# Performance work log

Measured on AMD Instinct MI355X. Metric: run time of the kernel, lower is better.

The kernel has to match this reference:

```python
import jax, jax.numpy as jnp
import numpy as np

P_DROP = 0.1
NTYPES = 8
DROP_KEY = jax.random.key(42)


def _dropout(h, i):
    # deterministic training-mode dropout, mask fixed by layer index
    keep = jax.random.bernoulli(jax.random.fold_in(DROP_KEY, i), 1.0 - P_DROP, h.shape)
    return jnp.where(keep, h / (1.0 - P_DROP), 0.0).astype(h.dtype)


def _func_conv(h, src, dst, types, convW, convb, act):
    # gather src features along edges, mean-aggregate onto dst nodes,
    # then apply a per-gate-type linear transform.
    n_out = types.shape[0]
    msg = h[src]                                                  # [E, d]
    agg = jax.ops.segment_sum(msg, dst, num_segments=n_out)       # [n_out, d]
    deg = jax.ops.segment_sum(jnp.ones((src.shape[0],), h.dtype), dst,
                              num_segments=n_out)
    agg = agg / jnp.maximum(deg, 1.0)[:, None]
    out = jnp.zeros((n_out, convW.shape[2]), h.dtype)
    for t in range(convW.shape[0]):                                # ntypes is small & fixed
        mask = (types == t).astype(h.dtype)[:, None]
        out = out + (agg * mask) @ convW[t]
    out = out + convb[types]
    return jax.nn.relu(out) if act else out


def setup_inputs() -> dict:
    key = jax.random.key(0)
    ks = jax.random.split(key, 16)
    N0, N1, N2, N3 = 400_000, 200_000, 100_000, 50_000
    E0, E1, E2 = 1_600_000, 800_000, 400_000
    d, dout = 128, 64
    inp = {
        "features": jax.random.normal(ks[0], (N0, d), jnp.float32),
        "src0": jax.random.randint(ks[1], (E0,), 0, N0),
        "dst0": jax.random.randint(ks[2], (E0,), 0, N1),
        "types1": jax.random.randint(ks[3], (N1,), 0, NTYPES),
        "src1": jax.random.randint(ks[4], (E1,), 0, N1),
        "dst1": jax.random.randint(ks[5], (E1,), 0, N2),
        "types2": jax.random.randint(ks[6], (N2,), 0, NTYPES),
        "src2": jax.random.randint(ks[7], (E2,), 0, N2),
        "dst2": jax.random.randint(ks[8], (E2,), 0, N3),
        "types3": jax.random.randint(ks[9], (N3,), 0, NTYPES),
        # learned params
        "convW": jax.random.normal(ks[10], (NTYPES, d, d), jnp.float32) / np.sqrt(d),
        "convb": jnp.zeros((NTYPES, d), jnp.float32),
        "fcW": jax.random.normal(ks[11], (d, dout), jnp.float32) / np.sqrt(d),
        "fcb": jnp.zeros((dout,), jnp.float32),
    }
    return inp


def reference(features, src0, dst0, types1, src1, dst1, types2,
              src2, dst2, types3, convW, convb, fcW, fcb):
    blocks = [(src0, dst0, types1), (src1, dst1, types2), (src2, dst2, types3)]
    depth = len(blocks)
    h = features
    for i, (s, dst, t) in enumerate(blocks):
        if i != 0:
            h = _dropout(h, i)
        h = _func_conv(h, s, dst, t, convW, convb, act=(i != depth - 1))
    h = h @ fcW + fcb   # hidden_dim != out_dim -> fc_out applied
    return h            # squeeze(1) is a no-op for out_dim > 1
```

## Files before the change

### kernel.cpp

```cpp
#include <hip/hip_runtime.h>
#include <cstdint>
#include <cstddef>

__host__ __device__ inline void tf2x32(uint32_t k0, uint32_t k1,
                                       uint32_t x0, uint32_t x1,
                                       uint32_t* o0, uint32_t* o1)
{
    uint32_t ks2 = k0 ^ k1 ^ 0x1BD11BDAu;
    x0 += k0; x1 += k1;
#define TF_R(r) do { x0 += x1; x1 = (x1 << (r)) | (x1 >> (32 - (r))); x1 ^= x0; } while (0)
    TF_R(13); TF_R(15); TF_R(26); TF_R(6);
    x0 += k1;  x1 += ks2 + 1u;
    TF_R(17); TF_R(29); TF_R(16); TF_R(24);
    x0 += ks2; x1 += k0 + 2u;
    TF_R(13); TF_R(15); TF_R(26); TF_R(6);
    x0 += k0;  x1 += k1 + 3u;
    TF_R(17); TF_R(29); TF_R(16); TF_R(24);
    x0 += k1;  x1 += ks2 + 4u;
    TF_R(13); TF_R(15); TF_R(26); TF_R(6);
    x0 += ks2; x1 += k0 + 5u;
#undef TF_R
    *o0 = x0; *o1 = x1;
}

__device__ inline float drop_scale(uint32_t fk0, uint32_t fk1, uint32_t idx)
{
    uint32_t o0, o1;
    tf2x32(fk0, fk1, 0u, idx, &o0, &o1);
    uint32_t bits = o0 ^ o1;
    float u = __uint_as_float((bits >> 9) | 0x3f800000u) - 1.0f;
    return (u < 0.9f) ? (1.0f / 0.9f) : 0.0f;
}

__device__ inline ushort bf16_rn(float f)
{
    uint32_t u = __float_as_uint(f);
    u += 0x7fffu + ((u >> 16) & 1u);
    return (ushort)(u >> 16);
}
__device__ inline float bf16_f(ushort h) { return __uint_as_float(((uint32_t)h) << 16); }
__device__ inline uint32_t pack2bf(float a, float b)
{
    return (uint32_t)bf16_rn(a) | ((uint32_t)bf16_rn(b) << 16);
}
__device__ inline float bflo(uint32_t u) { return __uint_as_float(u << 16); }
__device__ inline float bfhi(uint32_t u) { return __uint_as_float(u & 0xffff0000u); }

typedef __attribute__((ext_vector_type(8))) short bf16x8;
typedef __attribute__((ext_vector_type(4))) float f32x4;

__global__ __launch_bounds__(256) void fcvt_kernel(
    const float4* __restrict__ in, uint2* __restrict__ out, long long n4)
{
    long long stride = (long long)gridDim.x * 256;
    for (long long i = blockIdx.x * 256LL + threadIdx.x; i < n4; i += stride) {
        float4 v = in[i];
        out[i] = make_uint2(pack2bf(v.x, v.y), pack2bf(v.z, v.w));
    }
}

__global__ __launch_bounds__(256) void prep_all_kernel(
    const float* __restrict__ convW, const float* __restrict__ convb,
    const float* __restrict__ fcW, const float* __restrict__ fcb,
    ushort* __restrict__ WThi, ushort* __restrict__ WTlo,
    ushort* __restrict__ WfThi, ushort* __restrict__ WfTlo,
    float* __restrict__ bfb)
{
    __shared__ float F[128 * 64];
    int t = blockIdx.x, tid = threadIdx.x;
    #pragma unroll
    for (int it = 0; it < 8; ++it) {
        int idx4 = (it * 256 + tid) * 4;
        *(float4*)&F[idx4] = *(const float4*)&fcW[idx4];
    }
    __syncthreads();

    {
        const float* S = convW + (size_t)t * 16384;
        ushort* DH = WThi + (size_t)t * 16384;
        ushort* DL = WTlo + (size_t)t * 16384;
        for (int idx = tid; idx < 16384; idx += 256) {
            int k = idx >> 7, c = idx & 127;
            float v = S[idx];
            ushort hi = bf16_rn(v);
            ushort lo = bf16_rn(v - bf16_f(hi));
            int pos = c * 128 + ((((k >> 3) ^ (c & 15)) << 3) | (k & 7));
            DH[pos] = hi; DL[pos] = lo;
        }
    }

    {
        int r = tid >> 1, cb = (tid & 1) * 32;
        const float* Wrow = convW + (size_t)t * 16384 + (size_t)r * 128;
        float acc[32];
        #pragma unroll
        for (int c = 0; c < 32; ++c) acc[c] = 0.f;
        for (int k = 0; k < 128; ++k) {
            float w = Wrow[k];
            #pragma unroll
            for (int c = 0; c < 32; ++c) acc[c] += w * F[k * 64 + cb + c];
        }
        ushort* FH = WfThi + (size_t)t * 8192;
        ushort* FL = WfTlo + (size_t)t * 8192;
        int swzr = (r & 7);
        #pragma unroll
        for (int c = 0; c < 32; ++c) {
            int col = cb + c;
            float v = acc[c];
            ushort hi = bf16_rn(v);
            ushort lo = bf16_rn(v - bf16_f(hi));
            int pos = col * 128 + ((((r >> 3) ^ (col & 15)) << 3) | swzr);
            FH[pos] = hi; FL[pos] = lo;
        }
    }

    if (tid < 64) {
        float a = fcb[tid];
        const float* bt = convb + (size_t)t * 128;
        for (int k = 0; k < 128; ++k) a += bt[k] * F[k * 64 + tid];
        bfb[(size_t)t * 64 + tid] = a;
    }
}

#define EPB 4096

__global__ __launch_bounds__(256) void hist_all_kernel(
    const int* __restrict__ d0, const int* __restrict__ d1, const int* __restrict__ d2,
    const int* __restrict__ t1, const int* __restrict__ t2, const int* __restrict__ t3,
    int E0, int E1, int E2, int N1, int N2, int N3,
    int nb0, int nb1, int nb2, int nblk0, int nblk1, int nblk2,
    int cO0, int cO1, int cO2,
    uint32_t* __restrict__ tot, uint32_t* __restrict__ tcnt,
    uint32_t* __restrict__ cnt)
{
    int L = blockIdx.y;
    int tid = threadIdx.x;
    if (L < 3) {
        const int* dst = L == 0 ? d0 : (L == 1 ? d1 : d2);
        int E  = L == 0 ? E0 : (L == 1 ? E1 : E2);
        int NB = L == 0 ? nb0 : (L == 1 ? nb1 : nb2);
        int nblk = L == 0 ? nblk0 : (L == 1 ? nblk1 : nblk2);
        int gO = L == 0 ? 0 : (L == 1 ? nb0 : nb0 + nb1);
        int cO = L == 0 ? cO0 : (L == 1 ? cO1 : cO2);
        if ((int)blockIdx.x >= nblk) return;
        __shared__ uint32_t lh[256];
        lh[tid] = 0;
        __syncthreads();
        int base = blockIdx.x * EPB;
        for (int i = tid; i < EPB; i += 256) {
            int e = base + i;
            if (e < E) atomicAdd(&lh[((uint32_t)dst[e]) >> 10], 1u);
        }
        __syncthreads();
        if (tid < NB) {
            cnt[cO + (size_t)blockIdx.x * NB + tid] = lh[tid];
            if (lh[tid]) atomicAdd(&tot[gO + tid], lh[tid]);
        }
    } else {
        int totalN = N1 + N2 + N3;
        if ((int)blockIdx.x * 256 >= totalN) return;
        __shared__ uint32_t lh[24];
        if (tid < 24) lh[tid] = 0;
        __syncthreads();
        int i = blockIdx.x * 256 + tid;
        if (i < N1) atomicAdd(&lh[t1[i]], 1u);
        else if (i < N1 + N2) atomicAdd(&lh[8 + t2[i - N1]], 1u);
        else if (i < totalN) atomicAdd(&lh[16 + t3[i - N1 - N2]], 1u);
        __syncthreads();
        if (tid < 24 && lh[tid]) atomicAdd(&tcnt[tid], lh[tid]);
    }
}

__global__ __launch_bounds__(512) void scan_all_kernel(
    const uint32_t* __restrict__ tot, uint32_t* __restrict__ bo,
    uint32_t* __restrict__ bcur, uint32_t* __restrict__ rowptr3,
    const uint32_t* __restrict__ tcnt, int* __restrict__ boff,
    uint32_t* __restrict__ tcur, int* __restrict__ order3,
    int nb0, int nb1, int nb2, int N1, int N2, int N3,
    int r1, int r2, int no1p, int no2p)
{
    __shared__ uint32_t bol[348];
    __shared__ int pB[27];
    __shared__ int cnts[24];
    int t = threadIdx.x;
    int TB = nb0 + nb1 + nb2;
    if (t < 3) {
        int nb = t == 0 ? nb0 : (t == 1 ? nb1 : nb2);
        int g0 = t == 0 ? 0 : (t == 1 ? nb0 : nb0 + nb1);
        int gi0 = g0 + t;
        uint32_t run = 0;
        for (int i = 0; i < nb; ++i) { bol[gi0 + i] = run; run += tot[g0 + i]; }
        bol[gi0 + nb] = run;
        int rp = t == 0 ? 0 : (t == 1 ? r1 : r2);
        int N = t == 0 ? N1 : (t == 1 ? N2 : N3);
        rowptr3[rp + N] = run;
    }
    if (t == 3) {
        for (int L = 0; L < 3; ++L) {
            int a = 0;
            for (int ty = 0; ty < 8; ++ty) {
                pB[L * 9 + ty] = a;
                int c = (int)tcnt[L * 8 + ty];
                cnts[L * 8 + ty] = c;
                tcur[L * 8 + ty] = (uint32_t)a;
                a += (c + 127) & ~127;
            }
            pB[L * 9 + 8] = a;
        }
    }
    __syncthreads();
    for (int i = t; i < TB + 3; i += 512) bo[i] = bol[i];
    if (t < TB) {
        int layer = t < nb0 ? 0 : (t < nb0 + nb1 ? 1 : 2);
        bcur[t] = bol[t + layer];
    }
    if (t < 27) boff[t] = pB[t];
    if (t < 24) {
        int L = t >> 3, ty = t & 7;
        int noff = L == 0 ? 0 : (L == 1 ? no1p : no2p);
        int s = pB[L * 9 + ty] + cnts[t];
        int e2 = pB[L * 9 + ty + 1];
        for (int k = s; k < e2; ++k) order3[noff + k] = -1;
    }
}

__global__ __launch_bounds__(256) void scatter_all_kernel(
    const int* __restrict__ s0, const int* __restrict__ d0,
    const int* __restrict__ s1, const int* __restrict__ d1,
    const int* __restrict__ s2, const int* __restrict__ d2,
    const int* __restrict__ t1, const int* __restrict__ t2, const int* __restrict__ t3,
    int E0, int E1, int E2, int N1, int N2, int N3,
    int nb0, int nb1, int nb2, int nblk0, int nblk1, int nblk2,
    int cO0, int cO1, int cO2, const uint32_t* __restrict__ cnt,
    uint32_t* __restrict__ bcur, uint32_t* __restrict__ pairs,
    uint32_t* __restrict__ tcur, int* __restrict__ order3, int no1p, int no2p)
{
    int L = blockIdx.y;
    int tid = threadIdx.x;
    if (L < 3) {
        const int* src = L == 0 ? s0 : (L == 1 ? s1 : s2);
        const int* dst = L == 0 ? d0 : (L == 1 ? d1 : d2);
        int E  = L == 0 ? E0 : (L == 1 ? E1 : E2);
        int NB = L == 0 ? nb0 : (L == 1 ? nb1 : nb2);
        int nblk = L == 0 ? nblk0 : (L == 1 ? nblk1 : nblk2);
        int gO = L == 0 ? 0 : (L == 1 ? nb0 : nb0 + nb1);
        int cO = L == 0 ? cO0 : (L == 1 ? cO1 : cO2);
        uint32_t* pr = pairs + (L == 0 ? 0 : (L == 1 ? E0 : E0 + E1));
        if ((int)blockIdx.x >= nblk) return;

        __shared__ uint32_t lbase[256], rank[256];
        rank[tid] = 0;
        __syncthreads();
        if (tid < NB) {
            uint32_t c = cnt[cO + (size_t)blockIdx.x * NB + tid];
            if (c) lbase[tid] = atomicAdd(&bcur[gO + tid], c);
        }
        __syncthreads();
        int base = blockIdx.x * EPB;
        for (int i = tid; i < EPB; i += 256) {
            int e = base + i;
            if (e < E) {
                uint32_t d = (uint32_t)dst[e];
                uint32_t bk = d >> 10;
                uint32_t r = atomicAdd(&rank[bk], 1u);
                pr[lbase[bk] + r] = ((d & 1023u) << 22) | (uint32_t)src[e];
            }
        }
    } else {
        int totalN = N1 + N2 + N3;
        if ((int)blockIdx.x * 256 >= totalN) return;
        __shared__ uint32_t lh[24], lbase[24];
        if (tid < 24) lh[tid] = 0;
        __syncthreads();
        int i = blockIdx.x * 256 + tid;
        int slot = -1, idx = 0; uint32_t r = 0;
        if (i < N1) { idx = i; slot = t1[idx]; }
        else if (i < N1 + N2) { idx = i - N1; slot = 8 + t2[idx]; }
        else if (i < totalN) { idx = i - N1 - N2; slot = 16 + t3[idx]; }
        if (slot >= 0) r = atomicAdd(&lh[slot], 1u);
        __syncthreads();
        if (tid < 24 && lh[tid]) lbase[tid] = atomicAdd(&tcur[tid], lh[tid]);
        __syncthreads();
        if (slot >= 0) {
            int noff = slot < 8 ? 0 : (slot < 16 ? no1p : no2p);
            order3[noff + lbase[slot] + r] = idx;
        }
    }
}

__global__ __launch_bounds__(256) void bfill_kernel(
    const uint32_t* __restrict__ bo, const uint32_t* __restrict__ pairs,
    int* __restrict__ elist3, uint32_t* __restrict__ rowptr3,
    int nb0, int nb1, int nb2, int N1, int N2, int N3,
    int E0, int E1, int r1, int r2)
{
    __shared__ uint32_t hist[1024];
    __shared__ uint32_t cur[1024];
    __shared__ uint32_t psum[256];
    int g = blockIdx.x, tid = threadIdx.x;
    int layer, lb, N, Eoff, rp;
    if (g < nb0) { layer = 0; lb = g; N = N1; Eoff = 0; rp = 0; }
    else if (g < nb0 + nb1) { layer = 1; lb = g - nb0; N = N2; Eoff = E0; rp = r1; }
    else { layer = 2; lb = g - nb0 - nb1; N = N3; Eoff = E0 + E1; rp = r2; }
    uint32_t off = bo[g + layer], end = bo[g + layer + 1];
    int nodeBase = lb << 10;
    int nodesIn = N - nodeBase; if (nodesIn > 1024) nodesIn = 1024;

    #pragma unroll
    for (int i = 0; i < 4; ++i) hist[tid * 4 + i] = 0;
    __syncthreads();
    for (uint32_t e = off + tid; e < end; e += 256)
        atomicAdd(&hist[pairs[Eoff + e] >> 22], 1u);
    __syncthreads();

    uint32_t x[4]; uint32_t s = 0;
    #pragma unroll
    for (int i = 0; i < 4; ++i) { x[i] = hist[tid * 4 + i]; s += x[i]; }
    psum[tid] = s; __syncthreads();
    uint32_t inc = s;
    #pragma unroll
    for (int o = 1; o < 256; o <<= 1) {
        uint32_t y = (tid >= o) ? psum[tid - o] : 0u;
        __syncthreads();
        inc += y; psum[tid] = inc;
        __syncthreads();
    }
    uint32_t run = off + inc - s;
    #pragma unroll
    for (int i = 0; i < 4; ++i) { cur[tid * 4 + i] = run; run += x[i]; }
    __syncthreads();

    for (int i = tid; i < nodesIn; i += 256)
        rowptr3[rp + nodeBase + i] = cur[i];
    __syncthreads();

    for (uint32_t e = off + tid; e < end; e += 256) {
        uint32_t pk = pairs[Eoff + e];
        uint32_t pos = atomicAdd(&cur[pk >> 22], 1u);
        elist3[Eoff + pos] = (int)(pk & 0x3FFFFFu);
    }
}

__global__ __launch_bounds__(256) void aggregate_kernel(
    const uint32_t* __restrict__ hbf, const uint32_t* __restrict__ rowptr,
    const int* __restrict__ elist, uint32_t* __restrict__ agghi,
    uint32_t* __restrict__ agglo, int nout)
{
    int wid = threadIdx.x >> 6, lane = threadIdx.x & 63;
    int n0 = blockIdx.x * 8 + wid * 2;
    if (n0 >= nout) return;
    int n1 = n0 + 1;
    bool v1 = (n1 < nout);
    uint32_t b0 = rowptr[n0], e0 = rowptr[n0 + 1];
    uint32_t b1 = v1 ? rowptr[n1] : 0u, e1 = v1 ? rowptr[n1 + 1] : 0u;
    const uint32_t* base = hbf + lane;
    float a0x = 0.f, a0y = 0.f, a1x = 0.f, a1y = 0.f;
    uint32_t i0 = b0, i1 = b1;

    while (i0 + 8 <= e0 && i1 + 8 <= e1) {
        uint32_t u[8], w[8];
        #pragma unroll
        for (int k = 0; k < 8; ++k) u[k] = base[(size_t)elist[i0 + k] * 64];
        #pragma unroll
        for (int k = 0; k < 8; ++k) w[k] = base[(size_t)elist[i1 + k] * 64];
        #pragma unroll
        for (int k = 0; k < 8; ++k) { a0x += bflo(u[k]); a0y += bfhi(u[k]); }
        #pragma unroll
        for (int k = 0; k < 8; ++k) { a1x += bflo(w[k]); a1y += bfhi(w[k]); }
        i0 += 8; i1 += 8;
    }
    while (i0 + 4 <= e0 && i1 + 4 <= e1) {
        uint32_t u[4], w[4];
        #pragma unroll
        for (int k = 0; k < 4; ++k) u[k] = base[(size_t)elist[i0 + k] * 64];
        #pragma unroll
        for (int k = 0; k < 4; ++k) w[k] = base[(size_t)elist[i1 + k] * 64];
        #pragma unroll
        for (int k = 0; k < 4; ++k) { a0x += bflo(u[k]); a0y += bfhi(u[k]); }
        #pragma unroll
        for (int k = 0; k < 4; ++k) { a1x += bflo(w[k]); a1y += bfhi(w[k]); }
        i0 += 4; i1 += 4;
    }
    while (i0 + 4 <= e0) {
        uint32_t u[4];
        #pragma unroll
        for (int k = 0; k < 4; ++k) u[k] = base[(size_t)elist[i0 + k] * 64];
        #pragma unroll
        for (int k = 0; k < 4; ++k) { a0x += bflo(u[k]); a0y += bfhi(u[k]); }
        i0 += 4;
    }
    while (i1 + 4 <= e1) {
        uint32_t w[4];
        #pragma unroll
        for (int k = 0; k < 4; ++k) w[k] = base[(size_t)elist[i1 + k] * 64];
        #pragma unroll
        for (int k = 0; k < 4; ++k) { a1x += bflo(w[k]); a1y += bfhi(w[k]); }
        i1 += 4;
    }
    for (; i0 < e0; ++i0) {
        uint32_t u = base[(size_t)elist[i0] * 64];
        a0x += bflo(u); a0y += bfhi(u);
    }
    for (; i1 < e1; ++i1) {
        uint32_t w = base[(size_t)elist[i1] * 64];
        a1x += bflo(w); a1y += bfhi(w);
    }

    float sc0 = 1.0f / fmaxf((float)(e0 - b0), 1.0f);
    a0x *= sc0; a0y *= sc0;
    ushort hx = bf16_rn(a0x); ushort lx = bf16_rn(a0x - bf16_f(hx));
    ushort hy = bf16_rn(a0y); ushort ly = bf16_rn(a0y - bf16_f(hy));
    agghi[(size_t)n0 * 64 + lane] = (uint32_t)hx | ((uint32_t)hy << 16);
    agglo[(size_t)n0 * 64 + lane] = (uint32_t)lx | ((uint32_t)ly << 16);
    if (v1) {
        float sc1 = 1.0f / fmaxf((float)(e1 - b1), 1.0f);
        a1x *= sc1; a1y *= sc1;
        ushort hx1 = bf16_rn(a1x); ushort lx1 = bf16_rn(a1x - bf16_f(hx1));
        ushort hy1 = bf16_rn(a1y); ushort ly1 = bf16_rn(a1y - bf16_f(hy1));
        agghi[(size_t)n1 * 64 + lane] = (uint32_t)hx1 | ((uint32_t)hy1 << 16);
        agglo[(size_t)n1 * 64 + lane] = (uint32_t)lx1 | ((uint32_t)ly1 << 16);
    }
}

template<int DOUT, bool RELU, bool DROP, bool OUTBF>
__global__ __launch_bounds__(512) void mfma_gemm_kernel(
    const uint32_t* __restrict__ agghi, const uint32_t* __restrict__ agglo,
    const int* __restrict__ order, const int* __restrict__ off,
    const ushort* __restrict__ WThi, const ushort* __restrict__ WTlo,
    const float* __restrict__ bias8, void* __restrict__ houtv,
    uint32_t fk0, uint32_t fk1)
{
    __shared__ ushort WH[DOUT * 128];
    __shared__ ushort WL[DOUT * 128];
    __shared__ int ND[128];

    int b0 = blockIdx.x * 128;
    if (b0 >= off[8]) return;
    int t = 0;
    #pragma unroll
    for (int u = 1; u < 8; ++u) if (b0 >= off[u]) ++t;
    int tid = threadIdx.x;

    if (tid < 128) ND[tid] = order[b0 + tid];

    {
        const float4* sh = (const float4*)(WThi + (size_t)t * DOUT * 128);
        const float4* sl = (const float4*)(WTlo + (size_t)t * DOUT * 128);
        float4* dh = (float4*)WH; float4* dl = (float4*)WL;
        #pragma unroll
        for (int it = 0; it < DOUT * 16 / 512; ++it) {
            int c = it * 512 + tid;
            dh[c] = sh[c]; dl[c] = sl[c];
        }
    }
    __syncthreads();

    int wid = tid >> 6, lane = tid & 63;
    int r15 = lane & 15, q = lane >> 4;
    int arow = wid * 16 + r15;
    int nd_a = ND[arow];

    const bf16x8* gh = (const bf16x8*)agghi;
    const bf16x8* gl = (const bf16x8*)agglo;
    bf16x8 zero8 = (bf16x8){0, 0, 0, 0, 0, 0, 0, 0};
    bf16x8 ahv[4], alv[4];
    {
        size_t rowb = (size_t)(nd_a < 0 ? 0 : nd_a) * 16;
        #pragma unroll
        for (int ks = 0; ks < 4; ++ks) {
            size_t ix = rowb + (q + ks * 4);
            ahv[ks] = (nd_a >= 0) ? gh[ix] : zero8;
            alv[ks] = (nd_a >= 0) ? gl[ix] : zero8;
        }
    }

    constexpr int NF = DOUT / 16;
    f32x4 acc[NF];
    #pragma unroll
    for (int i = 0; i < NF; ++i) acc[i] = (f32x4){0.f, 0.f, 0.f, 0.f};

    const bf16x8* WHp = (const bf16x8*)WH;
    const bf16x8* WLp = (const bf16x8*)WL;

    #pragma unroll
    for (int ks = 0; ks < 4; ++ks) {
        int sch = (q + ks * 4) ^ r15;
        bf16x8 ah = ahv[ks];
        bf16x8 al = alv[ks];
        #pragma unroll
        for (int nf = 0; nf < NF; ++nf) {
            int col = nf * 16 + r15;
            bf16x8 bh = WHp[col * 16 + sch];
            bf16x8 bl = WLp[col * 16 + sch];
            acc[nf] = __builtin_amdgcn_mfma_f32_16x16x32_bf16(ah, bh, acc[nf], 0, 0, 0);
            acc[nf] = __builtin_amdgcn_mfma_f32_16x16x32_bf16(ah, bl, acc[nf], 0, 0, 0);
            acc[nf] = __builtin_amdgcn_mfma_f32_16x16x32_bf16(al, bh, acc[nf], 0, 0, 0);
        }
    }

    int ndr[4];
    #pragma unroll
    for (int r = 0; r < 4; ++r) ndr[r] = ND[wid * 16 + q * 4 + r];
    const float* bptr = bias8 + (size_t)t * DOUT;

    #pragma unroll
    for (int nf = 0; nf < NF; ++nf) {
        int col = nf * 16 + r15;
        float bv = bptr[col];
        float vr[4];
        #pragma unroll
        for (int r = 0; r < 4; ++r) {
            float v = acc[nf][r] + bv;
            if (RELU) v = fmaxf(v, 0.f);
            if (DROP) {
                int nd = ndr[r] < 0 ? 0 : ndr[r];
                v *= drop_scale(fk0, fk1, (uint32_t)nd * 128u + (uint32_t)col);
            }
            vr[r] = v;
        }
        if (OUTBF) {
            uint32_t* hb = (uint32_t*)houtv;
            #pragma unroll
            for (int r = 0; r < 4; ++r) {
                float w = __shfl_xor(vr[r], 1, 64);
                if ((lane & 1) == 0 && ndr[r] >= 0)
                    hb[(size_t)ndr[r] * (DOUT / 2) + (col >> 1)] = pack2bf(vr[r], w);
            }
        } else {
            float* ho = (float*)houtv;
            #pragma unroll
            for (int r = 0; r < 4; ++r)
                if (ndr[r] >= 0) ho[(size_t)ndr[r] * DOUT + col] = vr[r];
        }
    }
}

extern "C" void kernel_launch(void* const* d_in, const int* in_sizes, int n_in,
                              void* d_out, int out_size, void* d_ws, size_t ws_size,
                              hipStream_t stream)
{
    const float* features = (const float*)d_in[0];
    const int*   src0 = (const int*)d_in[1];
    const int*   dst0 = (const int*)d_in[2];
    const int*   types1 = (const int*)d_in[3];
    const int*   src1 = (const int*)d_in[4];
    const int*   dst1 = (const int*)d_in[5];
    const int*   types2 = (const int*)d_in[6];
    const int*   src2 = (const int*)d_in[7];
    const int*   dst2 = (const int*)d_in[8];
    const int*   types3 = (const int*)d_in[9];
    const float* convW = (const float*)d_in[10];
    const float* convb = (const float*)d_in[11];
    const float* fcW   = (const float*)d_in[12];
    const float* fcb   = (const float*)d_in[13];

    int N0 = in_sizes[0] / 128;
    int E0 = in_sizes[1], N1 = in_sizes[3];
    int E1 = in_sizes[4], N2 = in_sizes[6];
    int E2 = in_sizes[7], N3 = in_sizes[9];
    int totalN = N1 + N2 + N3;
    int totalE = E0 + E1 + E2;
    int r1 = N1 + 1, r2 = N1 + 1 + N2 + 1;
    int no1p = N1 + 1024, no2p = no1p + N2 + 1024;
    int maxN = N1 > N2 ? N1 : N2; if (N3 > maxN) maxN = N3;

    int nb0 = (N1 + 1023) >> 10, nb1 = (N2 + 1023) >> 10, nb2 = (N3 + 1023) >> 10;
    int TB = nb0 + nb1 + nb2;
    int nblk0 = (E0 + EPB - 1) / EPB, nblk1 = (E1 + EPB - 1) / EPB, nblk2 = (E2 + EPB - 1) / EPB;
    int nblkMax = nblk0 > nblk1 ? nblk0 : nblk1; if (nblk2 > nblkMax) nblkMax = nblk2;
    int nblkT = (totalN + 255) / 256;
    int gx = nblkMax > nblkT ? nblkMax : nblkT;
    int cO0 = 0;
    int cO1 = cO0 + nblk0 * nb0;
    int cO2 = cO1 + nblk1 * nb1;
    int cntEntries = cO2 + nblk2 * nb2;

    char* ws = (char*)d_ws;
    size_t woff = 0;
    auto alloc = [&](size_t bytes) -> void* {
        void* p = ws + woff;
        woff = (woff + bytes + 255) & ~(size_t)255;
        return p;
    };
    uint32_t* fbf     = (uint32_t*)alloc((size_t)N0 * 64 * 4);
    uint32_t* hbf     = fbf;
    uint32_t* aggHi   = (uint32_t*)alloc((size_t)maxN * 64 * 4);
    uint32_t* pairs   = aggHi;
    uint32_t* aggLo   = (uint32_t*)alloc((size_t)maxN * 64 * 4);
    uint32_t* rowptr3 = (uint32_t*)alloc((size_t)(totalN + 3) * 4);
    int*      elist3  = (int*)alloc((size_t)totalE * 4);
    int*      order3  = (int*)alloc((size_t)(totalN + 3 * 1024) * 4);
    uint32_t* cnt     = (uint32_t*)alloc((size_t)cntEntries * 4);
    uint32_t* tot     = (uint32_t*)alloc((size_t)(TB + 8 + 24) * 4);
    uint32_t* tcnt    = tot + TB + 8;
    uint32_t* bcur    = (uint32_t*)alloc((size_t)(TB + 8) * 4);
    uint32_t* bo      = (uint32_t*)alloc((size_t)(TB + 3) * 4);
    int*      boff    = (int*)alloc(27 * 4);
    uint32_t* tcur    = (uint32_t*)alloc(24 * 4);
    float*    bfb     = (float*)alloc((size_t)8 * 64 * 4);
    ushort*   WThi    = (ushort*)alloc((size_t)8 * 128 * 128 * 2);
    ushort*   WTlo    = (ushort*)alloc((size_t)8 * 128 * 128 * 2);
    ushort*   WfThi   = (ushort*)alloc((size_t)8 * 64 * 128 * 2);
    ushort*   WfTlo   = (ushort*)alloc((size_t)8 * 64 * 128 * 2);
    (void)ws_size; (void)n_in; (void)out_size;

    fcvt_kernel<<<4096, 256, 0, stream>>>(
        (const float4*)features, (uint2*)fbf, (long long)N0 * 32);
    prep_all_kernel<<<8, 256, 0, stream>>>(
        convW, convb, fcW, fcb, WThi, WTlo, WfThi, WfTlo, bfb);

    hipMemsetAsync(tot, 0, (size_t)(TB + 8 + 24) * 4, stream);
    hist_all_kernel<<<dim3(gx, 4), 256, 0, stream>>>(
        dst0, dst1, dst2, types1, types2, types3,
        E0, E1, E2, N1, N2, N3, nb0, nb1, nb2, nblk0, nblk1, nblk2,
        cO0, cO1, cO2, tot, tcnt, cnt);
    scan_all_kernel<<<1, 512, 0, stream>>>(
        tot, bo, bcur, rowptr3, tcnt, boff, tcur, order3,
        nb0, nb1, nb2, N1, N2, N3, r1, r2, no1p, no2p);
    scatter_all_kernel<<<dim3(gx, 4), 256, 0, stream>>>(
        src0, dst0, src1, dst1, src2, dst2, types1, types2, types3,
        E0, E1, E2, N1, N2, N3, nb0, nb1, nb2, nblk0, nblk1, nblk2,
        cO0, cO1, cO2, cnt, bcur, pairs, tcur, order3, no1p, no2p);
    bfill_kernel<<<TB, 256, 0, stream>>>(bo, pairs, elist3, rowptr3,
        nb0, nb1, nb2, N1, N2, N3, E0, E1, r1, r2);

    uint32_t fk1a, fk1b, fk2a, fk2b;
    tf2x32(0u, 42u, 0u, 1u, &fk1a, &fk1b);
    tf2x32(0u, 42u, 0u, 2u, &fk2a, &fk2b);

    aggregate_kernel<<<(N1 + 7) / 8, 256, 0, stream>>>(
        fbf, rowptr3, elist3, aggHi, aggLo, N1);
    mfma_gemm_kernel<128, true, true, true><<<(N1 + 127) / 128 + 8, 512, 0, stream>>>(
        aggHi, aggLo, order3, boff, WThi, WTlo, convb, hbf, fk1a, fk1b);

    aggregate_kernel<<<(N2 + 7) / 8, 256, 0, stream>>>(
        hbf, rowptr3 + r1, elist3 + E0, aggHi, aggLo, N2);
    mfma_gemm_kernel<128, true, true, true><<<(N2 + 127) / 128 + 8, 512, 0, stream>>>(
        aggHi, aggLo, order3 + no1p, boff + 9, WThi, WTlo, convb, hbf, fk2a, fk2b);

    aggregate_kernel<<<(N3 + 7) / 8, 256, 0, stream>>>(
        hbf, rowptr3 + r2, elist3 + E0 + E1, aggHi, aggLo, N3);
    mfma_gemm_kernel<64, false, false, false><<<(N3 + 127) / 128 + 8, 512, 0, stream>>>(
        aggHi, aggLo, order3 + no2p, boff + 18, WfThi, WfTlo, bfb, d_out, 0u, 0u);
}
```

Measured before the change: 538.5 us.

## Fuse prep kernels into histogram launch and precompute dropout bitmasks in aggregation

Result: faster. 494.1 us (-8.3%).

```diff
diff --git a/kernel.cpp b/kernel.cpp
--- a/kernel.cpp
+++ b/kernel.cpp
@@ -23,13 +23,13 @@
     *o0 = x0; *o1 = x1;
 }
 
-__device__ inline float drop_scale(uint32_t fk0, uint32_t fk1, uint32_t idx)
+__device__ inline bool drop_keep(uint32_t fk0, uint32_t fk1, uint32_t idx)
 {
     uint32_t o0, o1;
     tf2x32(fk0, fk1, 0u, idx, &o0, &o1);
     uint32_t bits = o0 ^ o1;
     float u = __uint_as_float((bits >> 9) | 0x3f800000u) - 1.0f;
-    return (u < 0.9f) ? (1.0f / 0.9f) : 0.0f;
+    return u < 0.9f;
 }
 
 __device__ inline ushort bf16_rn(float f)
@@ -49,82 +49,15 @@
 typedef __attribute__((ext_vector_type(8))) short bf16x8;
 typedef __attribute__((ext_vector_type(4))) float f32x4;
 
-__global__ __launch_bounds__(256) void fcvt_kernel(
-    const float4* __restrict__ in, uint2* __restrict__ out, long long n4)
-{
-    long long stride = (long long)gridDim.x * 256;
-    for (long long i = blockIdx.x * 256LL + threadIdx.x; i < n4; i += stride) {
-        float4 v = in[i];
-        out[i] = make_uint2(pack2bf(v.x, v.y), pack2bf(v.z, v.w));
-    }
-}
-
-__global__ __launch_bounds__(256) void prep_all_kernel(
+#define EPB 4096
+
+__global__ __launch_bounds__(256) void phase1_kernel(
+    const float4* __restrict__ fin, uint2* __restrict__ fout, long long n4,
     const float* __restrict__ convW, const float* __restrict__ convb,
     const float* __restrict__ fcW, const float* __restrict__ fcb,
     ushort* __restrict__ WThi, ushort* __restrict__ WTlo,
     ushort* __restrict__ WfThi, ushort* __restrict__ WfTlo,
-    float* __restrict__ bfb)
-{
-    __shared__ float F[128 * 64];
-    int t = blockIdx.x, tid = threadIdx.x;
-    #pragma unroll
-    for (int it = 0; it < 8; ++it) {
-        int idx4 = (it * 256 + tid) * 4;
-        *(float4*)&F[idx4] = *(const float4*)&fcW[idx4];
-    }
-    __syncthreads();
-
-    {
-        const float* S = convW + (size_t)t * 16384;
-        ushort* DH = WThi + (size_t)t * 16384;
-        ushort* DL = WTlo + (size_t)t * 16384;
-        for (int idx = tid; idx < 16384; idx += 256) {
-            int k = idx >> 7, c = idx & 127;
-            float v = S[idx];
-            ushort hi = bf16_rn(v);
-            ushort lo = bf16_rn(v - bf16_f(hi));
-            int pos = c * 128 + ((((k >> 3) ^ (c & 15)) << 3) | (k & 7));
-            DH[pos] = hi; DL[pos] = lo;
-        }
-    }
-
-    {
-        int r = tid >> 1, cb = (tid & 1) * 32;
-        const float* Wrow = convW + (size_t)t * 16384 + (size_t)r * 128;
-        float acc[32];
-        #pragma unroll
-        for (int c = 0; c < 32; ++c) acc[c] = 0.f;
-        for (int k = 0; k < 128; ++k) {
-            float w = Wrow[k];
-            #pragma unroll
-            for (int c = 0; c < 32; ++c) acc[c] += w * F[k * 64 + cb + c];
-        }
-        ushort* FH = WfThi + (size_t)t * 8192;
-        ushort* FL = WfTlo + (size_t)t * 8192;
-        int swzr = (r & 7);
-        #pragma unroll
-        for (int c = 0; c < 32; ++c) {
-            int col = cb + c;
-            float v = acc[c];
-            ushort hi = bf16_rn(v);
-            ushort lo = bf16_rn(v - bf16_f(hi));
-            int pos = col * 128 + ((((r >> 3) ^ (col & 15)) << 3) | swzr);
-            FH[pos] = hi; FL[pos] = lo;
-        }
-    }
-
-    if (tid < 64) {
-        float a = fcb[tid];
-        const float* bt = convb + (size_t)t * 128;
-        for (int k = 0; k < 128; ++k) a += bt[k] * F[k * 64 + tid];
-        bfb[(size_t)t * 64 + tid] = a;
-    }
-}
-
-#define EPB 4096
-
-__global__ __launch_bounds__(256) void hist_all_kernel(
+    float* __restrict__ bfb,
     const int* __restrict__ d0, const int* __restrict__ d1, const int* __restrict__ d2,
     const int* __restrict__ t1, const int* __restrict__ t2, const int* __restrict__ t3,
     int E0, int E1, int E2, int N1, int N2, int N3,
@@ -133,8 +66,11 @@
     uint32_t* __restrict__ tot, uint32_t* __restrict__ tcnt,
     uint32_t* __restrict__ cnt)
 {
+    __shared__ float F[128 * 64];
+    uint32_t* lh = (uint32_t*)F;
     int L = blockIdx.y;
     int tid = threadIdx.x;
+
     if (L < 3) {
         const int* dst = L == 0 ? d0 : (L == 1 ? d1 : d2);
         int E  = L == 0 ? E0 : (L == 1 ? E1 : E2);
@@ -143,7 +79,6 @@
         int gO = L == 0 ? 0 : (L == 1 ? nb0 : nb0 + nb1);
         int cO = L == 0 ? cO0 : (L == 1 ? cO1 : cO2);
         if ((int)blockIdx.x >= nblk) return;
-        __shared__ uint32_t lh[256];
         lh[tid] = 0;
         __syncthreads();
         int base = blockIdx.x * EPB;
@@ -156,10 +91,9 @@
             cnt[cO + (size_t)blockIdx.x * NB + tid] = lh[tid];
             if (lh[tid]) atomicAdd(&tot[gO + tid], lh[tid]);
         }
-    } else {
+    } else if (L == 3) {
         int totalN = N1 + N2 + N3;
         if ((int)blockIdx.x * 256 >= totalN) return;
-        __shared__ uint32_t lh[24];
         if (tid < 24) lh[tid] = 0;
         __syncthreads();
         int i = blockIdx.x * 256 + tid;
@@ -168,6 +102,65 @@
         else if (i < totalN) atomicAdd(&lh[16 + t3[i - N1 - N2]], 1u);
         __syncthreads();
         if (tid < 24 && lh[tid]) atomicAdd(&tcnt[tid], lh[tid]);
+    } else if (L == 4) {
+        long long stride = (long long)gridDim.x * 256;
+        for (long long i = blockIdx.x * 256LL + tid; i < n4; i += stride) {
+            float4 v = fin[i];
+            fout[i] = make_uint2(pack2bf(v.x, v.y), pack2bf(v.z, v.w));
+        }
+    } else {
+        if ((int)blockIdx.x >= 8) return;
+        int t = blockIdx.x;
+        #pragma unroll
+        for (int it = 0; it < 8; ++it) {
+            int idx4 = (it * 256 + tid) * 4;
+            *(float4*)&F[idx4] = *(const float4*)&fcW[idx4];
+        }
+        __syncthreads();
+
+        {
+            const float* S = convW + (size_t)t * 16384;
+            ushort* DH = WThi + (size_t)t * 16384;
+            ushort* DL = WTlo + (size_t)t * 16384;
+            for (int idx = tid; idx < 16384; idx += 256) {
+                int k = idx >> 7, c = idx & 127;
+                float v = S[idx];
+                ushort hi = bf16_rn(v);
+                ushort lo = bf16_rn(v - bf16_f(hi));
+                int pos = c * 128 + ((((k >> 3) ^ (c & 15)) << 3) | (k & 7));
+                DH[pos] = hi; DL[pos] = lo;
+            }
+        }
+        {
+            int r = tid >> 1, cb = (tid & 1) * 32;
+            const float* Wrow = convW + (size_t)t * 16384 + (size_t)r * 128;
+            float acc[32];
+            #pragma unroll
+            for (int c = 0; c < 32; ++c) acc[c] = 0.f;
+            for (int k = 0; k < 128; ++k) {
+                float w = Wrow[k];
+                #pragma unroll
+                for (int c = 0; c < 32; ++c) acc[c] += w * F[k * 64 + cb + c];
+            }
+            ushort* FH = WfThi + (size_t)t * 8192;
+            ushort* FL = WfTlo + (size_t)t * 8192;
+            int swzr = (r & 7);
+            #pragma unroll
+            for (int c = 0; c < 32; ++c) {
+                int col = cb + c;
+                float v = acc[c];
+                ushort hi = bf16_rn(v);
+                ushort lo = bf16_rn(v - bf16_f(hi));
+                int pos = col * 128 + ((((r >> 3) ^ (col & 15)) << 3) | swzr);
+                FH[pos] = hi; FL[pos] = lo;
+            }
+        }
+        if (tid < 64) {
+            float a = fcb[tid];
+            const float* bt = convb + (size_t)t * 128;
+            for (int k = 0; k < 128; ++k) a += bt[k] * F[k * 64 + tid];
+            bfb[(size_t)t * 64 + tid] = a;
+        }
     }
 }
 
@@ -344,7 +337,8 @@
 __global__ __launch_bounds__(256) void aggregate_kernel(
     const uint32_t* __restrict__ hbf, const uint32_t* __restrict__ rowptr,
     const int* __restrict__ elist, uint32_t* __restrict__ agghi,
-    uint32_t* __restrict__ agglo, int nout)
+    uint32_t* __restrict__ agglo, uint32_t* __restrict__ maskbuf,
+    uint32_t fk0, uint32_t fk1, int do_drop, int nout)
 {
     int wid = threadIdx.x >> 6, lane = threadIdx.x & 63;
     int n0 = blockIdx.x * 8 + wid * 2;
@@ -420,6 +414,21 @@
         agghi[(size_t)n1 * 64 + lane] = (uint32_t)hx1 | ((uint32_t)hy1 << 16);
         agglo[(size_t)n1 * 64 + lane] = (uint32_t)lx1 | ((uint32_t)ly1 << 16);
     }
+
+    if (do_drop) {
+        unsigned long long mA = __ballot(drop_keep(fk0, fk1, (uint32_t)n0 * 128u + lane));
+        unsigned long long mB = __ballot(drop_keep(fk0, fk1, (uint32_t)n0 * 128u + 64u + lane));
+        if (lane == 0)
+            *(uint4*)&maskbuf[(size_t)n0 * 4] = make_uint4(
+                (uint32_t)mA, (uint32_t)(mA >> 32), (uint32_t)mB, (uint32_t)(mB >> 32));
+        if (v1) {
+            unsigned long long mC = __ballot(drop_keep(fk0, fk1, (uint32_t)n1 * 128u + lane));
+            unsigned long long mD = __ballot(drop_keep(fk0, fk1, (uint32_t)n1 * 128u + 64u + lane));
+            if (lane == 0)
+                *(uint4*)&maskbuf[(size_t)n1 * 4] = make_uint4(
+                    (uint32_t)mC, (uint32_t)(mC >> 32), (uint32_t)mD, (uint32_t)(mD >> 32));
+        }
+    }
 }
 
 template<int DOUT, bool RELU, bool DROP, bool OUTBF>
@@ -428,7 +437,7 @@
     const int* __restrict__ order, const int* __restrict__ off,
     const ushort* __restrict__ WThi, const ushort* __restrict__ WTlo,
     const float* __restrict__ bias8, void* __restrict__ houtv,
-    uint32_t fk0, uint32_t fk1)
+    const uint32_t* __restrict__ maskbuf)
 {
     __shared__ ushort WH[DOUT * 128];
     __shared__ ushort WL[DOUT * 128];
@@ -501,6 +510,14 @@
     int ndr[4];
     #pragma unroll
     for (int r = 0; r < 4; ++r) ndr[r] = ND[wid * 16 + q * 4 + r];
+    uint4 mrow[4];
+    if (DROP) {
+        #pragma unroll
+        for (int r = 0; r < 4; ++r) {
+            int nd = ndr[r] < 0 ? 0 : ndr[r];
+            mrow[r] = *(const uint4*)&maskbuf[(size_t)nd * 4];
+        }
+    }
     const float* bptr = bias8 + (size_t)t * DOUT;
 
     #pragma unroll
@@ -513,8 +530,9 @@
             float v = acc[nf][r] + bv;
             if (RELU) v = fmaxf(v, 0.f);
             if (DROP) {
-                int nd = ndr[r] < 0 ? 0 : ndr[r];
-                v *= drop_scale(fk0, fk1, (uint32_t)nd * 128u + (uint32_t)col);
+                const uint32_t* mw = (const uint32_t*)&mrow[r];
+                uint32_t m = mw[nf >> 1];
+                v = ((m >> (col & 31)) & 1u) ? v * (1.0f / 0.9f) : 0.0f;
             }
             vr[r] = v;
         }
@@ -570,6 +588,7 @@
     int nblkMax = nblk0 > nblk1 ? nblk0 : nblk1; if (nblk2 > nblkMax) nblkMax = nblk2;
     int nblkT = (totalN + 255) / 256;
     int gx = nblkMax > nblkT ? nblkMax : nblkT;
+    int gxF = gx > 1024 ? gx : 1024;
     int cO0 = 0;
     int cO1 = cO0 + nblk0 * nb0;
     int cO2 = cO1 + nblk1 * nb1;
@@ -587,6 +606,7 @@
     uint32_t* aggHi   = (uint32_t*)alloc((size_t)maxN * 64 * 4);
     uint32_t* pairs   = aggHi;
     uint32_t* aggLo   = (uint32_t*)alloc((size_t)maxN * 64 * 4);
+    uint32_t* maskbuf = (uint32_t*)alloc((size_t)maxN * 4 * 4);
     uint32_t* rowptr3 = (uint32_t*)alloc((size_t)(totalN + 3) * 4);
     int*      elist3  = (int*)alloc((size_t)totalE * 4);
     int*      order3  = (int*)alloc((size_t)(totalN + 3 * 1024) * 4);
@@ -604,13 +624,10 @@
     ushort*   WfTlo   = (ushort*)alloc((size_t)8 * 64 * 128 * 2);
     (void)ws_size; (void)n_in; (void)out_size;
 
-    fcvt_kernel<<<4096, 256, 0, stream>>>(
-        (const float4*)features, (uint2*)fbf, (long long)N0 * 32);
-    prep_all_kernel<<<8, 256, 0, stream>>>(
-        convW, convb, fcW, fcb, WThi, WTlo, WfThi, WfTlo, bfb);
-
     hipMemsetAsync(tot, 0, (size_t)(TB + 8 + 24) * 4, stream);
-    hist_all_kernel<<<dim3(gx, 4), 256, 0, stream>>>(
+    phase1_kernel<<<dim3(gxF, 6), 256, 0, stream>>>(
+        (const float4*)features, (uint2*)fbf, (long long)N0 * 32,
+        convW, convb, fcW, fcb, WThi, WTlo, WfThi, WfTlo, bfb,
         dst0, dst1, dst2, types1, types2, types3,
         E0, E1, E2, N1, N2, N3, nb0, nb1, nb2, nblk0, nblk1, nblk2,
         cO0, cO1, cO2, tot, tcnt, cnt);
@@ -629,17 +646,17 @@
     tf2x32(0u, 42u, 0u, 2u, &fk2a, &fk2b);
 
     aggregate_kernel<<<(N1 + 7) / 8, 256, 0, stream>>>(
-        fbf, rowptr3, elist3, aggHi, aggLo, N1);
+        fbf, rowptr3, elist3, aggHi, aggLo, maskbuf, fk1a, fk1b, 1, N1);
     mfma_gemm_kernel<128, true, true, true><<<(N1 + 127) / 128 + 8, 512, 0, stream>>>(
-        aggHi, aggLo, order3, boff, WThi, WTlo, convb, hbf, fk1a, fk1b);
+        aggHi, aggLo, order3, boff, WThi, WTlo, convb, hbf, maskbuf);
 
     aggregate_kernel<<<(N2 + 7) / 8, 256, 0, stream>>>(
-        hbf, rowptr3 + r1, elist3 + E0, aggHi, aggLo, N2);
+        hbf, rowptr3 + r1, elist3 + E0, aggHi, aggLo, maskbuf, fk2a, fk2b, 1, N2);
     mfma_gemm_kernel<128, true, true, true><<<(N2 + 127) / 128 + 8, 512, 0, stream>>>(
-        aggHi, aggLo, order3 + no1p, boff + 9, WThi, WTlo, convb, hbf, fk2a, fk2b);
+        aggHi, aggLo, order3 + no1p, boff + 9, WThi, WTlo, convb, hbf, maskbuf);
 
     aggregate_kernel<<<(N3 + 7) / 8, 256, 0, stream>>>(
-        hbf, rowptr3 + r2, elist3 + E0 + E1, aggHi, aggLo, N3);
+        hbf, rowptr3 + r2, elist3 + E0 + E1, aggHi, aggLo, maskbuf, 0u, 0u, 0, N3);
     mfma_gemm_kernel<64, false, false, false><<<(N3 + 127) / 128 + 8, 512, 0, stream>>>(
-        aggHi, aggLo, order3 + no2p, boff + 18, WfThi, WfTlo, bfb, d_out, 0u, 0u);
-}
+        aggHi, aggLo, order3 + no2p, boff + 18, WfThi, WfTlo, bfb, d_out, nullptr);
+}
```
